# Kernel tuning notes

Measured on AMD Instinct MI355X. Metric: run time of the kernel, lower is better.

The kernel has to match this reference:

```python
import jax, jax.numpy as jnp
import numpy as np

EPS = 1e-06

def _feature_map(x):
    # elu_feature_map: phi(x) = elu(x) + 1  (strictly positive features)
    return jax.nn.elu(x) + 1.0

def setup_inputs() -> dict:
    key = jax.random.key(0)
    kq, kk, kv = jax.random.split(key, 3)
    N, L, H, D, M = 2, 2048, 8, 64, 64
    return {
        "queries": jax.random.normal(kq, (N, L, H, D), dtype=jnp.float32),
        "keys": jax.random.normal(kk, (N, L, H, D), dtype=jnp.float32),
        "values": jax.random.normal(kv, (N, L, H, M), dtype=jnp.float32),
    }

def reference(queries, keys, values):
    Q = _feature_map(queries)   # [N,L,H,D]
    K = _feature_map(keys)      # [N,L,H,D]
    # normalizer: Z_i = 1 / (Q_i . sum_{j<=i} K_j + eps)
    Z = 1.0 / (jnp.einsum('nlhi,nlhi->nlh', Q, jnp.cumsum(K, axis=1)) + EPS)
    # causal linear attention: S_i = sum_{j<=i} K_j outer V_j ; out_i = Q_i @ S_i
    S = jnp.cumsum(jnp.einsum('nlhd,nlhm->nlhdm', K, values), axis=1)  # [N,L,H,D,M]
    V = jnp.einsum('nlhd,nlhdm->nlhm', Q, S)
    return V * Z[:, :, :, None]
```

## Files before the change

### kernel.cpp

```cpp
#include <hip/hip_runtime.h>


namespace {
constexpr int N_ = 2, L_ = 2048, H_ = 8, D_ = 64, M_ = 64;
constexpr int C  = 64;
constexpr int G  = L_ / C;
constexpr int NH = N_ * H_;
constexpr int LDH = H_ * D_;
constexpr int STR = 68;
constexpr float EPS_ = 1e-6f;
}

__device__ __forceinline__ float phi(float x) {
    return x > 0.0f ? x + 1.0f : __expf(x);
}

__global__ __launch_bounds__(256, 4) void k_chunksum(
    const float* __restrict__ keys, const float* __restrict__ values,
    float* __restrict__ wsS, float* __restrict__ wsK)
{
    __shared__ __align__(16) float Ks[C * STR];
    __shared__ __align__(16) float Vs[C * STR];
    const int bid = blockIdx.x;
    const int g = bid % G, nh = bid / G;
    const int n = nh / H_, h = nh % H_;
    const int t = threadIdx.x;
    const size_t base = ((size_t)(n * L_ + g * C) * H_ + h) * D_;

#pragma unroll
    for (int r = 0; r < 4; ++r) {
        const int f = t + 256 * r;
        const int row = f >> 4, c = (f & 15) * 4;
        const size_t ga = base + (size_t)row * LDH + c;
        float4 kv = *(const float4*)(keys + ga);
        float4 vv = *(const float4*)(values + ga);
        *(float4*)&Ks[row * STR + c] =
            make_float4(phi(kv.x), phi(kv.y), phi(kv.z), phi(kv.w));
        *(float4*)&Vs[row * STR + c] = vv;
    }
    __syncthreads();

    const int d0 = (t >> 4) * 4, m0 = (t & 15) * 4;
    float acc[4][4] = {};
#pragma unroll 8
    for (int j = 0; j < C; ++j) {
        const float4 k4 = *(const float4*)&Ks[j * STR + d0];
        const float4 v4 = *(const float4*)&Vs[j * STR + m0];
        acc[0][0] = fmaf(k4.x, v4.x, acc[0][0]);
        acc[0][1] = fmaf(k4.x, v4.y, acc[0][1]);
        acc[0][2] = fmaf(k4.x, v4.z, acc[0][2]);
        acc[0][3] = fmaf(k4.x, v4.w, acc[0][3]);
        acc[1][0] = fmaf(k4.y, v4.x, acc[1][0]);
        acc[1][1] = fmaf(k4.y, v4.y, acc[1][1]);
        acc[1][2] = fmaf(k4.y, v4.z, acc[1][2]);
        acc[1][3] = fmaf(k4.y, v4.w, acc[1][3]);
        acc[2][0] = fmaf(k4.z, v4.x, acc[2][0]);
        acc[2][1] = fmaf(k4.z, v4.y, acc[2][1]);
        acc[2][2] = fmaf(k4.z, v4.z, acc[2][2]);
        acc[2][3] = fmaf(k4.z, v4.w, acc[2][3]);
        acc[3][0] = fmaf(k4.w, v4.x, acc[3][0]);
        acc[3][1] = fmaf(k4.w, v4.y, acc[3][1]);
        acc[3][2] = fmaf(k4.w, v4.z, acc[3][2]);
        acc[3][3] = fmaf(k4.w, v4.w, acc[3][3]);
    }
    float* Sc = wsS + (size_t)bid * (D_ * M_);
#pragma unroll
    for (int a = 0; a < 4; ++a)
        *(float4*)(Sc + (d0 + a) * M_ + m0) =
            make_float4(acc[a][0], acc[a][1], acc[a][2], acc[a][3]);

    if (t < D_) {
        float s = 0.f;
#pragma unroll
        for (int j = 0; j < C; ++j) s += Ks[j * STR + t];
        wsK[(size_t)bid * D_ + t] = s;
    }
}

__global__ __launch_bounds__(256) void k_scan(
    float* __restrict__ wsS, float* __restrict__ wsK)
{
    const int bid = blockIdx.x;
    const int nh = bid >> 2, q = bid & 3;
    const int t = threadIdx.x;

    float4 run = make_float4(0.f, 0.f, 0.f, 0.f);
    float* base = wsS + (size_t)nh * G * (D_ * M_) + q * 1024 + (size_t)t * 4;
#pragma unroll
    for (int g = 0; g < G; ++g) {
        float4* p = (float4*)(base + (size_t)g * (D_ * M_));
        const float4 v = *p;
        *p = run;
        run.x += v.x; run.y += v.y; run.z += v.z; run.w += v.w;
    }

    if (q == 0 && t < D_ / 4) {
        float4 rk = make_float4(0.f, 0.f, 0.f, 0.f);
        float* kb = wsK + (size_t)nh * G * D_ + (size_t)t * 4;
#pragma unroll
        for (int g = 0; g < G; ++g) {
            float4* p = (float4*)(kb + (size_t)g * D_);
            const float4 v = *p;
            *p = rk;
            rk.x += v.x; rk.y += v.y; rk.z += v.z; rk.w += v.w;
        }
    }
}

__global__ __launch_bounds__(256, 4) void k_out(
    const float* __restrict__ queries, const float* __restrict__ keys,
    const float* __restrict__ values, float* __restrict__ out,
    const float* __restrict__ wsS, const float* __restrict__ wsK)
{
    __shared__ __align__(16) float Qs[C * STR];
    __shared__ __align__(16) float KA[C * STR];
    __shared__ __align__(16) float Vs[C * STR];
    __shared__ float Zs[C];

    const int bid = blockIdx.x;
    const int g = bid % G, nh = bid / G;
    const int n = nh / H_, h = nh % H_;
    const int t = threadIdx.x;
    const size_t base = ((size_t)(n * L_ + g * C) * H_ + h) * D_;

#pragma unroll
    for (int r = 0; r < 4; ++r) {
        const int f = t + 256 * r;
        const int row = f >> 4, c = (f & 15) * 4;
        const size_t ga = base + (size_t)row * LDH + c;
        float4 qv = *(const float4*)(queries + ga);
        float4 kv = *(const float4*)(keys + ga);
        float4 vv = *(const float4*)(values + ga);
        *(float4*)&Qs[row * STR + c] =
            make_float4(phi(qv.x), phi(qv.y), phi(qv.z), phi(qv.w));
        *(float4*)&KA[row * STR + c] =
            make_float4(phi(kv.x), phi(kv.y), phi(kv.z), phi(kv.w));
        *(float4*)&Vs[row * STR + c] = vv;
    }
    __syncthreads();

    const int i0 = (t >> 4) * 4, jt = t & 15, m0 = (t & 15) * 4;

    float accA[4][4] = {};
#pragma unroll 4
    for (int d4 = 0; d4 < 16; ++d4) {
        const int dc = d4 * 4;
        const float4 k0 = *(const float4*)&KA[(jt     ) * STR + dc];
        const float4 k1 = *(const float4*)&KA[(jt + 16) * STR + dc];
        const float4 k2 = *(const float4*)&KA[(jt + 32) * STR + dc];
        const float4 k3 = *(const float4*)&KA[(jt + 48) * STR + dc];
#pragma unroll
        for (int a = 0; a < 4; ++a) {
            const float4 q4 = *(const float4*)&Qs[(i0 + a) * STR + dc];
            accA[a][0] += q4.x * k0.x + q4.y * k0.y + q4.z * k0.z + q4.w * k0.w;
            accA[a][1] += q4.x * k1.x + q4.y * k1.y + q4.z * k1.z + q4.w * k1.w;
            accA[a][2] += q4.x * k2.x + q4.y * k2.y + q4.z * k2.z + q4.w * k2.w;
            accA[a][3] += q4.x * k3.x + q4.y * k3.y + q4.z * k3.z + q4.w * k3.w;
        }
    }
    __syncthreads();

#pragma unroll
    for (int a = 0; a < 4; ++a) {
        const int i = i0 + a;
        KA[i * STR + jt]      = (jt      <= i) ? accA[a][0] : 0.f;
        KA[i * STR + jt + 16] = (jt + 16 <= i) ? accA[a][1] : 0.f;
        KA[i * STR + jt + 32] = (jt + 32 <= i) ? accA[a][2] : 0.f;
        KA[i * STR + jt + 48] = (jt + 48 <= i) ? accA[a][3] : 0.f;
    }
    __syncthreads();

    const float* kpref = wsK + (size_t)(nh * G + g) * D_;
    if (t < C) {
        float rs = 0.f, zd = 0.f;
#pragma unroll
        for (int d4 = 0; d4 < 16; ++d4) {
            const float4 a4 = *(const float4*)&KA[t * STR + d4 * 4];
            rs += (a4.x + a4.y) + (a4.z + a4.w);
            const float4 q4 = *(const float4*)&Qs[t * STR + d4 * 4];
            const float4 kp4 = *(const float4*)(kpref + d4 * 4);
            zd += q4.x * kp4.x + q4.y * kp4.y + q4.z * kp4.z + q4.w * kp4.w;
        }
        Zs[t] = 1.0f / (zd + rs + EPS_);
    }
    __syncthreads();

    const float* Sp = wsS + (size_t)(nh * G + g) * (D_ * M_);
    float acc[4][4] = {};

#pragma unroll 4
    for (int j4 = 0; j4 < 16; ++j4) {
        const int jc = j4 * 4;
        const float4 a0 = *(const float4*)&KA[(i0 + 0) * STR + jc];
        const float4 a1 = *(const float4*)&KA[(i0 + 1) * STR + jc];
        const float4 a2 = *(const float4*)&KA[(i0 + 2) * STR + jc];
        const float4 a3 = *(const float4*)&KA[(i0 + 3) * STR + jc];
#pragma unroll
        for (int jj = 0; jj < 4; ++jj) {
            const float4 v4 = *(const float4*)&Vs[(jc + jj) * STR + m0];
            const float w0 = jj == 0 ? a0.x : jj == 1 ? a0.y : jj == 2 ? a0.z : a0.w;
            const float w1 = jj == 0 ? a1.x : jj == 1 ? a1.y : jj == 2 ? a1.z : a1.w;
            const float w2 = jj == 0 ? a2.x : jj == 1 ? a2.y : jj == 2 ? a2.z : a2.w;
            const float w3 = jj == 0 ? a3.x : jj == 1 ? a3.y : jj == 2 ? a3.z : a3.w;
            acc[0][0] = fmaf(w0, v4.x, acc[0][0]);
            acc[0][1] = fmaf(w0, v4.y, acc[0][1]);
            acc[0][2] = fmaf(w0, v4.z, acc[0][2]);
            acc[0][3] = fmaf(w0, v4.w, acc[0][3]);
            acc[1][0] = fmaf(w1, v4.x, acc[1][0]);
            acc[1][1] = fmaf(w1, v4.y, acc[1][1]);
            acc[1][2] = fmaf(w1, v4.z, acc[1][2]);
            acc[1][3] = fmaf(w1, v4.w, acc[1][3]);
            acc[2][0] = fmaf(w2, v4.x, acc[2][0]);
            acc[2][1] = fmaf(w2, v4.y, acc[2][1]);
            acc[2][2] = fmaf(w2, v4.z, acc[2][2]);
            acc[2][3] = fmaf(w2, v4.w, acc[2][3]);
            acc[3][0] = fmaf(w3, v4.x, acc[3][0]);
            acc[3][1] = fmaf(w3, v4.y, acc[3][1]);
            acc[3][2] = fmaf(w3, v4.z, acc[3][2]);
            acc[3][3] = fmaf(w3, v4.w, acc[3][3]);
        }
    }

#pragma unroll 4
    for (int d4 = 0; d4 < 16; ++d4) {
        const int dc = d4 * 4;
        const float4 q0 = *(const float4*)&Qs[(i0 + 0) * STR + dc];
        const float4 q1 = *(const float4*)&Qs[(i0 + 1) * STR + dc];
        const float4 q2 = *(const float4*)&Qs[(i0 + 2) * STR + dc];
        const float4 q3 = *(const float4*)&Qs[(i0 + 3) * STR + dc];
#pragma unroll
        for (int dd = 0; dd < 4; ++dd) {
            const float4 s4 = *(const float4*)(Sp + (dc + dd) * M_ + m0);
            const float w0 = dd == 0 ? q0.x : dd == 1 ? q0.y : dd == 2 ? q0.z : q0.w;
            const float w1 = dd == 0 ? q1.x : dd == 1 ? q1.y : dd == 2 ? q1.z : q1.w;
            const float w2 = dd == 0 ? q2.x : dd == 1 ? q2.y : dd == 2 ? q2.z : q2.w;
            const float w3 = dd == 0 ? q3.x : dd == 1 ? q3.y : dd == 2 ? q3.z : q3.w;
            acc[0][0] = fmaf(w0, s4.x, acc[0][0]);
            acc[0][1] = fmaf(w0, s4.y, acc[0][1]);
            acc[0][2] = fmaf(w0, s4.z, acc[0][2]);
            acc[0][3] = fmaf(w0, s4.w, acc[0][3]);
            acc[1][0] = fmaf(w1, s4.x, acc[1][0]);
            acc[1][1] = fmaf(w1, s4.y, acc[1][1]);
            acc[1][2] = fmaf(w1, s4.z, acc[1][2]);
            acc[1][3] = fmaf(w1, s4.w, acc[1][3]);
            acc[2][0] = fmaf(w2, s4.x, acc[2][0]);
            acc[2][1] = fmaf(w2, s4.y, acc[2][1]);
            acc[2][2] = fmaf(w2, s4.z, acc[2][2]);
            acc[2][3] = fmaf(w2, s4.w, acc[2][3]);
            acc[3][0] = fmaf(w3, s4.x, acc[3][0]);
            acc[3][1] = fmaf(w3, s4.y, acc[3][1]);
            acc[3][2] = fmaf(w3, s4.z, acc[3][2]);
            acc[3][3] = fmaf(w3, s4.w, acc[3][3]);
        }
    }

#pragma unroll
    for (int a = 0; a < 4; ++a) {
        const float z = Zs[i0 + a];
        const size_t oa = ((size_t)(n * L_ + g * C + i0 + a) * H_ + h) * M_ + m0;
        *(float4*)(out + oa) =
            make_float4(acc[a][0] * z, acc[a][1] * z, acc[a][2] * z, acc[a][3] * z);
    }
}

extern "C" void kernel_launch(void* const* d_in, const int* in_sizes, int n_in,
                              void* d_out, int out_size, void* d_ws, size_t ws_size,
                              hipStream_t stream) {
    const float* q = (const float*)d_in[0];
    const float* k = (const float*)d_in[1];
    const float* v = (const float*)d_in[2];
    float* out = (float*)d_out;
    float* wsS = (float*)d_ws;
    float* wsK = wsS + (size_t)NH * G * D_ * M_;

    k_chunksum<<<dim3(NH * G), dim3(256), 0, stream>>>(k, v, wsS, wsK);
    k_scan<<<dim3(NH * 4), dim3(256), 0, stream>>>(wsS, wsK);
    k_out<<<dim3(NH * G), dim3(256), 0, stream>>>(q, k, v, out, wsS, wsK);
}
```

Measured before the change: 99.42 us.

## Fuse prefix scan into output kernel and skip masked causal tiles

Removes the separate scan kernel. Each output block now sums the chunk states of all earlier chunks directly from the workspace and stages the result in shared memory, along with the key prefix. It also skips the strictly upper-triangular intra-chunk work per wavefront and lowers the occupancy hint to make room for the larger shared memory. The cost is redundant O(G) global reads per block, up to 31 chunk states of 16KB each, plus load imbalance across chunks, all traded for one fewer launch and scan pass.

```diff
diff --git a/kernel.cpp b/kernel.cpp
--- a/kernel.cpp
+++ b/kernel.cpp
@@ -77,37 +77,7 @@
     }
 }
 
-__global__ __launch_bounds__(256) void k_scan(
-    float* __restrict__ wsS, float* __restrict__ wsK)
-{
-    const int bid = blockIdx.x;
-    const int nh = bid >> 2, q = bid & 3;
-    const int t = threadIdx.x;
-
-    float4 run = make_float4(0.f, 0.f, 0.f, 0.f);
-    float* base = wsS + (size_t)nh * G * (D_ * M_) + q * 1024 + (size_t)t * 4;
-#pragma unroll
-    for (int g = 0; g < G; ++g) {
-        float4* p = (float4*)(base + (size_t)g * (D_ * M_));
-        const float4 v = *p;
-        *p = run;
-        run.x += v.x; run.y += v.y; run.z += v.z; run.w += v.w;
-    }
-
-    if (q == 0 && t < D_ / 4) {
-        float4 rk = make_float4(0.f, 0.f, 0.f, 0.f);
-        float* kb = wsK + (size_t)nh * G * D_ + (size_t)t * 4;
-#pragma unroll
-        for (int g = 0; g < G; ++g) {
-            float4* p = (float4*)(kb + (size_t)g * D_);
-            const float4 v = *p;
-            *p = rk;
-            rk.x += v.x; rk.y += v.y; rk.z += v.z; rk.w += v.w;
-        }
-    }
-}
-
-__global__ __launch_bounds__(256, 4) void k_out(
+__global__ __launch_bounds__(256, 2) void k_out(
     const float* __restrict__ queries, const float* __restrict__ keys,
     const float* __restrict__ values, float* __restrict__ out,
     const float* __restrict__ wsS, const float* __restrict__ wsK)
@@ -115,12 +85,15 @@
     __shared__ __align__(16) float Qs[C * STR];
     __shared__ __align__(16) float KA[C * STR];
     __shared__ __align__(16) float Vs[C * STR];
+    __shared__ __align__(16) float SpL[D_ * M_];
+    __shared__ __align__(16) float KPs[C];
     __shared__ float Zs[C];
 
     const int bid = blockIdx.x;
     const int g = bid % G, nh = bid / G;
     const int n = nh / H_, h = nh % H_;
     const int t = threadIdx.x;
+    const int w = t >> 6;
     const size_t base = ((size_t)(n * L_ + g * C) * H_ + h) * D_;
 
 #pragma unroll
@@ -137,6 +110,26 @@
             make_float4(phi(kv.x), phi(kv.y), phi(kv.z), phi(kv.w));
         *(float4*)&Vs[row * STR + c] = vv;
     }
+
+    float4 ps0 = make_float4(0.f, 0.f, 0.f, 0.f);
+    float4 ps1 = ps0, ps2 = ps0, ps3 = ps0;
+    {
+        const float4* Sb = (const float4*)(wsS + (size_t)nh * G * (D_ * M_));
+#pragma unroll 2
+        for (int gp = 0; gp < g; ++gp) {
+            const float4* p = Sb + (size_t)gp * 1024 + t;
+            const float4 a = p[0], b = p[256], c = p[512], d = p[768];
+            ps0.x += a.x; ps0.y += a.y; ps0.z += a.z; ps0.w += a.w;
+            ps1.x += b.x; ps1.y += b.y; ps1.z += b.z; ps1.w += b.w;
+            ps2.x += c.x; ps2.y += c.y; ps2.z += c.z; ps2.w += c.w;
+            ps3.x += d.x; ps3.y += d.y; ps3.z += d.z; ps3.w += d.w;
+        }
+    }
+    float kp = 0.f;
+    if (t < C) {
+        const float* Kb = wsK + (size_t)nh * G * D_ + t;
+        for (int gp = 0; gp < g; ++gp) kp += Kb[(size_t)gp * D_];
+    }
     __syncthreads();
 
     const int i0 = (t >> 4) * 4, jt = t & 15, m0 = (t & 15) * 4;
@@ -145,17 +138,16 @@
 #pragma unroll 4
     for (int d4 = 0; d4 < 16; ++d4) {
         const int dc = d4 * 4;
-        const float4 k0 = *(const float4*)&KA[(jt     ) * STR + dc];
-        const float4 k1 = *(const float4*)&KA[(jt + 16) * STR + dc];
-        const float4 k2 = *(const float4*)&KA[(jt + 32) * STR + dc];
-        const float4 k3 = *(const float4*)&KA[(jt + 48) * STR + dc];
-#pragma unroll
-        for (int a = 0; a < 4; ++a) {
-            const float4 q4 = *(const float4*)&Qs[(i0 + a) * STR + dc];
-            accA[a][0] += q4.x * k0.x + q4.y * k0.y + q4.z * k0.z + q4.w * k0.w;
-            accA[a][1] += q4.x * k1.x + q4.y * k1.y + q4.z * k1.z + q4.w * k1.w;
-            accA[a][2] += q4.x * k2.x + q4.y * k2.y + q4.z * k2.z + q4.w * k2.w;
-            accA[a][3] += q4.x * k3.x + q4.y * k3.y + q4.z * k3.z + q4.w * k3.w;
+        const float4 q0 = *(const float4*)&Qs[(i0 + 0) * STR + dc];
+        const float4 q1 = *(const float4*)&Qs[(i0 + 1) * STR + dc];
+        const float4 q2 = *(const float4*)&Qs[(i0 + 2) * STR + dc];
+        const float4 q3 = *(const float4*)&Qs[(i0 + 3) * STR + dc];
+        for (int kk = 0; kk <= w; ++kk) {
+            const float4 k4 = *(const float4*)&KA[(jt + 16 * kk) * STR + dc];
+            accA[0][kk] += q0.x * k4.x + q0.y * k4.y + q0.z * k4.z + q0.w * k4.w;
+            accA[1][kk] += q1.x * k4.x + q1.y * k4.y + q1.z * k4.z + q1.w * k4.w;
+            accA[2][kk] += q2.x * k4.x + q2.y * k4.y + q2.z * k4.z + q2.w * k4.w;
+            accA[3][kk] += q3.x * k4.x + q3.y * k4.y + q3.z * k4.z + q3.w * k4.w;
         }
     }
     __syncthreads();
@@ -168,9 +160,16 @@
         KA[i * STR + jt + 32] = (jt + 32 <= i) ? accA[a][2] : 0.f;
         KA[i * STR + jt + 48] = (jt + 48 <= i) ? accA[a][3] : 0.f;
     }
-    __syncthreads();
-
-    const float* kpref = wsK + (size_t)(nh * G + g) * D_;
+    {
+        float4* Sl = (float4*)SpL;
+        Sl[t]       = ps0;
+        Sl[t + 256] = ps1;
+        Sl[t + 512] = ps2;
+        Sl[t + 768] = ps3;
+    }
+    if (t < C) KPs[t] = kp;
+    __syncthreads();
+
     if (t < C) {
         float rs = 0.f, zd = 0.f;
 #pragma unroll
@@ -178,18 +177,18 @@
             const float4 a4 = *(const float4*)&KA[t * STR + d4 * 4];
             rs += (a4.x + a4.y) + (a4.z + a4.w);
             const float4 q4 = *(const float4*)&Qs[t * STR + d4 * 4];
-            const float4 kp4 = *(const float4*)(kpref + d4 * 4);
+            const float4 kp4 = *(const float4*)&KPs[d4 * 4];
             zd += q4.x * kp4.x + q4.y * kp4.y + q4.z * kp4.z + q4.w * kp4.w;
         }
         Zs[t] = 1.0f / (zd + rs + EPS_);
     }
     __syncthreads();
 
-    const float* Sp = wsS + (size_t)(nh * G + g) * (D_ * M_);
     float acc[4][4] = {};
 
+    const int j4max = 4 * (w + 1);
 #pragma unroll 4
-    for (int j4 = 0; j4 < 16; ++j4) {
+    for (int j4 = 0; j4 < j4max; ++j4) {
         const int jc = j4 * 4;
         const float4 a0 = *(const float4*)&KA[(i0 + 0) * STR + jc];
         const float4 a1 = *(const float4*)&KA[(i0 + 1) * STR + jc];
@@ -230,7 +229,7 @@
         const float4 q3 = *(const float4*)&Qs[(i0 + 3) * STR + dc];
 #pragma unroll
         for (int dd = 0; dd < 4; ++dd) {
-            const float4 s4 = *(const float4*)(Sp + (dc + dd) * M_ + m0);
+            const float4 s4 = *(const float4*)&SpL[(dc + dd) * M_ + m0];
             const float w0 = dd == 0 ? q0.x : dd == 1 ? q0.y : dd == 2 ? q0.z : q0.w;
             const float w1 = dd == 0 ? q1.x : dd == 1 ? q1.y : dd == 2 ? q1.z : q1.w;
             const float w2 = dd == 0 ? q2.x : dd == 1 ? q2.y : dd == 2 ? q2.z : q2.w;
@@ -274,6 +273,5 @@
     float* wsK = wsS + (size_t)NH * G * D_ * M_;
 
     k_chunksum<<<dim3(NH * G), dim3(256), 0, stream>>>(k, v, wsS, wsK);
-    k_scan<<<dim3(NH * 4), dim3(256), 0, stream>>>(wsS, wsK);
     k_out<<<dim3(NH * G), dim3(256), 0, stream>>>(q, k, v, out, wsS, wsK);
 }
```

Result: slower. 115.2 us (+15.9%).
